# Performance work log

Measured on AMD Instinct MI355X. Metric: run time of the kernel, lower is better.

Reference implementation:

```python
import jax, jax.numpy as jnp
import numpy as np

D_MODEL = 1024
NUM_HEADS = 16
D_K = D_MODEL // NUM_HEADS
TEMPERATURE = 1.0
LN_EPS = 1e-5


def setup_inputs() -> dict:
    key = jax.random.key(0)
    ks = jax.random.split(key, 12)
    B, S, D = 4, 1024, D_MODEL
    w = lambda k: jax.random.normal(k, (D, D), dtype=jnp.float32) * 0.02
    b = lambda k: jax.random.normal(k, (D,), dtype=jnp.float32) * 0.01
    return {
        "query": jax.random.normal(ks[0], (B, S, D), dtype=jnp.float32),
        "key": jax.random.normal(ks[1], (B, S, D), dtype=jnp.float32),
        "value": jax.random.normal(ks[2], (B, S, D), dtype=jnp.float32),
        "wq": w(ks[3]), "bq": b(ks[4]),
        "wk": w(ks[5]), "bk": b(ks[6]),
        "wv": w(ks[7]), "bv": b(ks[8]),
        "wo": w(ks[9]), "bo": b(ks[10]),
        "temporal_bias": jax.random.normal(ks[11], (1, 1, NUM_HEADS, 1, 1), dtype=jnp.float32) * 0.01,
        "adaptive_temp": jnp.ones((1,), dtype=jnp.float32),
        "ln_gamma": jnp.ones((D,), dtype=jnp.float32),
        "ln_beta": jnp.zeros((D,), dtype=jnp.float32),
    }


def reference(query, key, value, wq, bq, wk, bk, wv, bv, wo, bo,
              temporal_bias, adaptive_temp, ln_gamma, ln_beta):
    B, S, D = query.shape
    H, dk = NUM_HEADS, D_K
    # QKV projections -> (B, H, S, dk)
    Q = (query @ wq.T + bq).reshape(B, S, H, dk).transpose(0, 2, 1, 3)
    K = (key @ wk.T + bk).reshape(B, S, H, dk).transpose(0, 2, 1, 3)
    V = (value @ wv.T + bv).reshape(B, S, H, dk).transpose(0, 2, 1, 3)
    scores = jnp.einsum('bhqd,bhkd->bhqk', Q, K) / jnp.sqrt(jnp.float32(dk))
    scores = scores / (TEMPERATURE * adaptive_temp)
    # torch broadcasting bug reproduced: (B,H,S,S) + (1,1,H,1,1) -> (1,B,H,S,S)
    scores5 = scores[None, ...] + temporal_bias  # (1, B, H, S, S)
    attn = jax.nn.softmax(scores5, axis=-1)      # (1, B, H, S, S)
    ctx5 = jnp.einsum('xbhqk,bhkd->xbhqd', attn, V)  # (1, B, H, S, dk)
    # torch: transpose(1,2) -> (1, H, B, S, dk), then view(B, S, D)
    ctx = jnp.swapaxes(ctx5, 1, 2).reshape(B, S, D)
    out = ctx @ wo.T + bo
    y = out + query
    mu = jnp.mean(y, axis=-1, keepdims=True)
    var = jnp.mean(jnp.square(y - mu), axis=-1, keepdims=True)
    out_ln = (y - mu) / jnp.sqrt(var + LN_EPS) * ln_gamma + ln_beta
    return out_ln, attn
```

## Files before the change

kernel.cpp:

```cpp
#include <hip/hip_runtime.h>
#include <math.h>

#define BB 4
#define SS 1024
#define DD 1024
#define HH 16
#define DKK 64
#define NN (BB*SS)
#define LN_EPS 1e-5f
#define QB 64
#define JB 64

typedef __attribute__((ext_vector_type(8))) short bf16x8;
typedef __attribute__((ext_vector_type(4))) float f32x4;
typedef __attribute__((address_space(3))) unsigned int lds_u32;
typedef const __attribute__((address_space(1))) unsigned int glb_u32;

static __device__ __forceinline__ unsigned short f2bf(float x){
    unsigned int u = __float_as_uint(x);
    u += 0x7fff + ((u >> 16) & 1);
    return (unsigned short)(u >> 16);
}
static __device__ __forceinline__ int swzp16(int r){
    return (r & 15) << 4;
}

__global__ __launch_bounds__(256)
void k_cvt_all(const float* __restrict__ q, const float* __restrict__ k,
               const float* __restrict__ v, const float* __restrict__ w0,
               const float* __restrict__ w1, const float* __restrict__ w2,
               const float* __restrict__ w3, unsigned short* __restrict__ xout,
               unsigned short* __restrict__ wout){
    const int bidx = blockIdx.x;
    const float* src; unsigned short* dst; size_t i;
    if (bidx < 6144) {
        const int z = bidx >> 11, bi = bidx & 2047;
        src = (z == 0) ? q : (z == 1) ? k : v;
        dst = xout + (size_t)z*NN*DD;
        i = ((size_t)bi*256 + threadIdx.x)*8;
    } else {
        const int z = (bidx - 6144) >> 9, bi = (bidx - 6144) & 511;
        src = (z == 0) ? w0 : (z == 1) ? w1 : (z == 2) ? w2 : w3;
        dst = wout + (size_t)z*DD*DD;
        i = ((size_t)bi*256 + threadIdx.x)*8;
    }
    float4 a = *reinterpret_cast<const float4*>(&src[i]);
    float4 b = *reinterpret_cast<const float4*>(&src[i+4]);
    int4 w;
    w.x = (int)((unsigned)f2bf(a.x) | ((unsigned)f2bf(a.y) << 16));
    w.y = (int)((unsigned)f2bf(a.z) | ((unsigned)f2bf(a.w) << 16));
    w.z = (int)((unsigned)f2bf(b.x) | ((unsigned)f2bf(b.y) << 16));
    w.w = (int)((unsigned)f2bf(b.z) | ((unsigned)f2bf(b.w) << 16));
    *reinterpret_cast<int4*>(&dst[i]) = w;
}

__global__ __launch_bounds__(256)
void k_gemmqkv(const unsigned short* __restrict__ Xb, const unsigned short* __restrict__ Wb,
               const float* __restrict__ b0, const float* __restrict__ b1,
               const float* __restrict__ b2, unsigned short* __restrict__ outb)
{
    __shared__ __align__(16) unsigned short Als[128*32];
    __shared__ __align__(16) unsigned short Bls[128*32];
    __shared__ __align__(16) unsigned short Cs[128*128];
    const int z = blockIdx.z;
    const unsigned short* X = Xb + (size_t)z*NN*DD;
    const unsigned short* W = Wb + (size_t)z*DD*DD;
    const float* bias = (z == 0) ? b0 : (z == 1) ? b1 : b2;
    unsigned short* out = outb + (size_t)z*NN*DD;

    const int row0 = blockIdx.x * 128;
    const int col0 = blockIdx.y * 128;
    const int t = threadIdx.x;
    const int w = t >> 6, l = t & 63;
    const int wr = w >> 1, wc = w & 1;

    f32x4 acc[4][4];
    #pragma unroll
    for (int m=0;m<4;++m)
        #pragma unroll
        for (int n=0;n<4;++n) acc[m][n] = (f32x4){0.f,0.f,0.f,0.f};

    const int srow  = l >> 2;
    const int skoff = (l & 3) * 8;

    for (int kt = 0; kt < DD; kt += 32) {
        #pragma unroll
        for (int i=0;i<2;++i) {
            const unsigned short* ga = X + (size_t)(row0 + w*32 + i*16 + srow)*DD + kt + skoff;
            const unsigned short* gb = W + (size_t)(col0 + w*32 + i*16 + srow)*DD + kt + skoff;
            __builtin_amdgcn_global_load_lds((glb_u32*)ga, (lds_u32*)&Als[(w*2+i)*512], 16, 0, 0);
            __builtin_amdgcn_global_load_lds((glb_u32*)gb, (lds_u32*)&Bls[(w*2+i)*512], 16, 0, 0);
        }
        __syncthreads();
        bf16x8 af[4], bfr[4];
        #pragma unroll
        for (int m=0;m<4;++m)
            af[m] = *reinterpret_cast<const bf16x8*>(&Als[(wr*64 + m*16 + (l&15))*32 + (l>>4)*8]);
        #pragma unroll
        for (int n=0;n<4;++n)
            bfr[n] = *reinterpret_cast<const bf16x8*>(&Bls[(wc*64 + n*16 + (l&15))*32 + (l>>4)*8]);
        __builtin_amdgcn_s_setprio(1);
        #pragma unroll
        for (int m=0;m<4;++m)
            #pragma unroll
            for (int n=0;n<4;++n)
                acc[m][n] = __builtin_amdgcn_mfma_f32_16x16x32_bf16(af[m], bfr[n], acc[m][n], 0, 0, 0);
        __builtin_amdgcn_s_setprio(0);
        __syncthreads();
    }

    if (z < 2) {
        #pragma unroll
        for (int m=0;m<4;++m){
            const int trb = wr*64 + m*16 + ((l>>4)<<2);
            #pragma unroll
            for (int n=0;n<4;++n){
                const int tc = wc*64 + n*16 + (l&15);
                const float bc = bias[col0 + tc];
                #pragma unroll
                for (int r=0;r<4;++r){
                    const int tr = trb + r;
                    *reinterpret_cast<unsigned short*>(
                        (char*)Cs + ((tr*256 + tc*2) ^ ((tr & 12) << 3))) = f2bf(acc[m][n][r] + bc);
                }
            }
        }
        __syncthreads();
        #pragma unroll
        for (int i=0;i<8;++i){
            const int slot = i*256 + t;
            const int r2 = slot >> 4, g = slot & 15;
            int4 v = *reinterpret_cast<const int4*>(
                (char*)Cs + ((r2*256 + g*16) ^ ((r2 & 12) << 3)));
            *reinterpret_cast<int4*>(&out[(size_t)(row0 + r2)*DD + col0 + g*8]) = v;
        }
    } else {
        #pragma unroll
        for (int m=0;m<4;++m){
            const int trb = wr*64 + m*16 + ((l>>4)<<2);
            #pragma unroll
            for (int n=0;n<4;++n){
                const int tc = wc*64 + n*16 + (l&15);
                const float bc = bias[col0 + tc];
                ushort4 pk;
                pk.x = f2bf(acc[m][n][0] + bc);
                pk.y = f2bf(acc[m][n][1] + bc);
                pk.z = f2bf(acc[m][n][2] + bc);
                pk.w = f2bf(acc[m][n][3] + bc);
                *reinterpret_cast<ushort4*>(
                    (char*)Cs + ((tc*256 + trb*2) ^ ((tc & 15) << 3))) = pk;
            }
        }
        __syncthreads();
        const int b = row0 >> 10;
        const int sbase = row0 & 1023;
        #pragma unroll
        for (int i=0;i<16;++i){
            const int cr = i*8 + (t>>5);
            const int ch = t & 31;
            ushort4 v = *reinterpret_cast<const ushort4*>(
                (char*)Cs + ((cr*256 + ch*8) ^ ((cr & 15) << 3)));
            const int gc = col0 + cr, h = gc >> 6, k = gc & 63;
            *reinterpret_cast<ushort4*>(
                &out[(((size_t)b*HH + h)*DKK + k)*SS + sbase + ch*4]) = v;
        }
    }
}

__global__ __launch_bounds__(512)
void k_attn(const unsigned short* __restrict__ Qb, const unsigned short* __restrict__ Kb,
            const unsigned short* __restrict__ Vtb, const float* __restrict__ at,
            float* __restrict__ attn, unsigned short* __restrict__ ctxb)
{
    __shared__ __align__(16) char SM[147456];
    __shared__ float rsbuf[QB];
    char* Ks   = SM;
    char* Vs   = SM + 8192;
    char* Pall = SM + 16384;
    float* scr = reinterpret_cast<float*>(SM);

    const int f   = blockIdx.x;
    const int wk2 = (f & 7)*128 + (f >> 3);
    const int bh  = wk2 >> 4;
    const int q0  = (wk2 & 15) * QB;
    const int b = bh >> 4, h = bh & 15;
    const int t = threadIdx.x, w = t >> 6, l = t & 63;
    const int g = w & 3;
    const int hf = w >> 2;
    const float alpha = 0.125f / at[0];

    const unsigned short* Qg = Qb  + (size_t)b*SS*DD + (size_t)h*64;
    const unsigned short* Kg = Kb  + (size_t)b*SS*DD + (size_t)h*64;
    const unsigned short* Vg = Vtb + (size_t)bh*DKK*SS;

    const int sj  = t >> 3;
    const int skc = (t & 7) * 8;

    const int qloc = g*16 + (l & 15);

    bf16x8 qf[2];
    #pragma unroll
    for (int ks = 0; ks < 2; ++ks)
        qf[ks] = *reinterpret_cast<const bf16x8*>(
            &Qg[(size_t)(q0 + qloc)*DD + ks*32 + (l>>4)*8]);

    {
        int4 kv = *reinterpret_cast<const int4*>(&Kg[(size_t)sj*DD + skc]);
        int4 vv = *reinterpret_cast<const int4*>(&Vg[(size_t)sj*SS + skc]);
        *reinterpret_cast<int4*>(Ks + ((sj*128 + skc*2) ^ ((sj & 7) << 4))) = kv;
        *reinterpret_cast<int4*>(Vs + ((sj*128 + skc*2) ^ ((sj & 7) << 4))) = vv;
    }
    __syncthreads();

    float srow = 0.f;
    f32x4 cacc[4];
    #pragma unroll
    for (int n = 0; n < 4; ++n) cacc[n] = (f32x4){0.f,0.f,0.f,0.f};

    for (int jt = 0; jt < SS; jt += JB) {
        const bool more = (jt + JB < SS);
        int4 knext, vnext;
        if (more) {
            knext = *reinterpret_cast<const int4*>(&Kg[(size_t)(jt + JB + sj)*DD + skc]);
            vnext = *reinterpret_cast<const int4*>(&Vg[(size_t)sj*SS + jt + JB + skc]);
        }
        f32x4 acc[2];
        #pragma unroll
        for (int n2 = 0; n2 < 2; ++n2) acc[n2] = (f32x4){0.f,0.f,0.f,0.f};
        __builtin_amdgcn_s_setprio(1);
        #pragma unroll
        for (int ks = 0; ks < 2; ++ks) {
            #pragma unroll
            for (int n2 = 0; n2 < 2; ++n2) {
                const int j = (2*hf + n2)*16 + (l & 15);
                bf16x8 kf = *reinterpret_cast<const bf16x8*>(
                    Ks + ((j*128 + (l>>4)*16 + ks*64) ^ ((j & 7) << 4)));
                acc[n2] = __builtin_amdgcn_mfma_f32_16x16x32_bf16(kf, qf[ks], acc[n2], 0, 0, 0);
            }
        }
        __builtin_amdgcn_s_setprio(0);
        #pragma unroll
        for (int n2 = 0; n2 < 2; ++n2) {
            float p0 = __expf(acc[n2][0]*alpha);
            float p1 = __expf(acc[n2][1]*alpha);
            float p2 = __expf(acc[n2][2]*alpha);
            float p3 = __expf(acc[n2][3]*alpha);
            srow += (p0 + p1) + (p2 + p3);
            int2 pk;
            pk.x = (int)((unsigned)f2bf(p0) | ((unsigned)f2bf(p1) << 16));
            pk.y = (int)((unsigned)f2bf(p2) | ((unsigned)f2bf(p3) << 16));
            *reinterpret_cast<int2*>(
                Pall + (size_t)qloc*2048 +
                ((jt*2 + (2*hf + n2)*32 + (l>>4)*8) ^ swzp16(qloc))) = pk;
        }
        __builtin_amdgcn_sched_barrier(0);
        asm volatile("s_waitcnt lgkmcnt(0)" ::: "memory");
        __builtin_amdgcn_sched_barrier(0);
        {
            bf16x8 pf = *reinterpret_cast<const bf16x8*>(
                Pall + (size_t)qloc*2048 +
                ((jt*2 + hf*64 + (l>>4)*16) ^ swzp16(qloc)));
            __builtin_amdgcn_s_setprio(1);
            #pragma unroll
            for (int n = 0; n < 4; ++n) {
                const int d = n*16 + (l & 15);
                bf16x8 vf = *reinterpret_cast<const bf16x8*>(
                    Vs + ((d*128 + (l>>4)*16 + hf*64) ^ ((d & 7) << 4)));
                cacc[n] = __builtin_amdgcn_mfma_f32_16x16x32_bf16(pf, vf, cacc[n], 0, 0, 0);
            }
            __builtin_amdgcn_s_setprio(0);
        }
        __syncthreads();
        if (more) {
            *reinterpret_cast<int4*>(Ks + ((sj*128 + skc*2) ^ ((sj & 7) << 4))) = knext;
            *reinterpret_cast<int4*>(Vs + ((sj*128 + skc*2) ^ ((sj & 7) << 4))) = vnext;
            __syncthreads();
        }
    }

    srow += __shfl_xor(srow, 16, 64);
    srow += __shfl_xor(srow, 32, 64);
    if ((l >> 4) == 0) scr[hf*64 + qloc] = srow;
    __syncthreads();
    const float sinv = 1.0f / (scr[qloc] + scr[64 + qloc]);
    if (hf == 0 && (l >> 4) == 0) rsbuf[qloc] = sinv;
    __syncthreads();

    if (hf == 0) {
        #pragma unroll
        for (int n = 0; n < 4; ++n)
            #pragma unroll
            for (int r = 0; r < 4; ++r)
                scr[(g*64 + l)*16 + n*4 + r] = cacc[n][r];
    }
    __syncthreads();
    if (hf == 1) {
        #pragma unroll
        for (int n = 0; n < 4; ++n) {
            const int d = n*16 + (l & 15);
            #pragma unroll
            for (int r = 0; r < 4; ++r) {
                const float v = (cacc[n][r] + scr[(g*64 + l)*16 + n*4 + r]) * sinv;
                const int q = q0 + g*16 + (l>>4)*4 + r;
                ctxb[(((size_t)h*BB + b)*SS + q)*DKK + d] = f2bf(v);
            }
        }
    }

    #pragma unroll
    for (int i = 0; i < 32; ++i) {
        const int seg = i*32 + (t >> 4);
        const int row = seg >> 4;
        const int cs  = (seg & 15)*64 + (t & 15)*4;
        const float rsv = rsbuf[row];
        int2 u = *reinterpret_cast<const int2*>(
            Pall + (size_t)row*2048 + ((cs*2) ^ swzp16(row)));
        f32x4 fv;
        fv.x = __uint_as_float(((unsigned)u.x) << 16)         * rsv;
        fv.y = __uint_as_float(((unsigned)u.x) & 0xffff0000u) * rsv;
        fv.z = __uint_as_float(((unsigned)u.y) << 16)         * rsv;
        fv.w = __uint_as_float(((unsigned)u.y) & 0xffff0000u) * rsv;
        __builtin_nontemporal_store(fv, reinterpret_cast<f32x4*>(
            &attn[((size_t)bh*SS + q0 + row)*SS + cs]));
    }
}

__global__ __launch_bounds__(256)
void k_gemmo(const unsigned short* __restrict__ X, const unsigned short* __restrict__ W,
             const float* __restrict__ bias, const float* __restrict__ resid,
             float* __restrict__ outf)
{
    __shared__ __align__(16) unsigned short Als[128*32];
    __shared__ __align__(16) unsigned short Bls[128*32];
    const int row0 = blockIdx.x * 128;
    const int col0 = blockIdx.y * 128;
    const int t = threadIdx.x;
    const int w = t >> 6, l = t & 63;
    const int wr = w >> 1, wc = w & 1;

    f32x4 acc[4][4];
    #pragma unroll
    for (int m=0;m<4;++m)
        #pragma unroll
        for (int n=0;n<4;++n) acc[m][n] = (f32x4){0.f,0.f,0.f,0.f};

    const int srow  = l >> 2;
    const int skoff = (l & 3) * 8;

    for (int kt = 0; kt < DD; kt += 32) {
        #pragma unroll
        for (int i=0;i<2;++i) {
            const unsigned short* ga = X + (size_t)(row0 + w*32 + i*16 + srow)*DD + kt + skoff;
            const unsigned short* gb = W + (size_t)(col0 + w*32 + i*16 + srow)*DD + kt + skoff;
            __builtin_amdgcn_global_load_lds((glb_u32*)ga, (lds_u32*)&Als[(w*2+i)*512], 16, 0, 0);
            __builtin_amdgcn_global_load_lds((glb_u32*)gb, (lds_u32*)&Bls[(w*2+i)*512], 16, 0, 0);
        }
        __syncthreads();
        bf16x8 af[4], bfr[4];
        #pragma unroll
        for (int m=0;m<4;++m)
            af[m] = *reinterpret_cast<const bf16x8*>(&Als[(wr*64 + m*16 + (l&15))*32 + (l>>4)*8]);
        #pragma unroll
        for (int n=0;n<4;++n)
            bfr[n] = *reinterpret_cast<const bf16x8*>(&Bls[(wc*64 + n*16 + (l&15))*32 + (l>>4)*8]);
        __builtin_amdgcn_s_setprio(1);
        #pragma unroll
        for (int m=0;m<4;++m)
            #pragma unroll
            for (int n=0;n<4;++n)
                acc[m][n] = __builtin_amdgcn_mfma_f32_16x16x32_bf16(af[m], bfr[n], acc[m][n], 0, 0, 0);
        __builtin_amdgcn_s_setprio(0);
        __syncthreads();
    }

    #pragma unroll
    for (int m=0;m<4;++m){
        const int grow_base = row0 + wr*64 + m*16 + ((l>>4)<<2);
        #pragma unroll
        for (int n=0;n<4;++n){
            const int col = col0 + wc*64 + n*16 + (l&15);
            const float bc = bias[col];
            #pragma unroll
            for (int r=0;r<4;++r){
                const int row = grow_base + r;
                outf[(size_t)row*DD + col] = acc[m][n][r] + bc + resid[(size_t)row*DD + col];
            }
        }
    }
}

__global__ __launch_bounds__(256)
void k_ln(const float* __restrict__ y, const float* __restrict__ g,
          const float* __restrict__ be, float* __restrict__ out)
{
    const int row = blockIdx.x;
    const int t = threadIdx.x;
    float4 v = *reinterpret_cast<const float4*>(&y[(size_t)row*DD + t*4]);
    float s  = v.x + v.y + v.z + v.w;
    float ss = v.x*v.x + v.y*v.y + v.z*v.z + v.w*v.w;
    #pragma unroll
    for (int off = 32; off > 0; off >>= 1) {
        s  += __shfl_xor(s,  off, 64);
        ss += __shfl_xor(ss, off, 64);
    }
    __shared__ float red[8];
    const int lane = t & 63, wid = t >> 6;
    if (lane == 0) { red[wid] = s; red[4+wid] = ss; }
    __syncthreads();
    const float S1 = red[0]+red[1]+red[2]+red[3];
    const float S2 = red[4]+red[5]+red[6]+red[7];
    const float mu  = S1 * (1.0f/DD);
    const float var = fmaxf(S2 * (1.0f/DD) - mu*mu, 0.0f);
    const float rstd = rsqrtf(var + LN_EPS);
    float4 gv = *reinterpret_cast<const float4*>(&g[t*4]);
    float4 bv = *reinterpret_cast<const float4*>(&be[t*4]);
    float4 o;
    o.x = (v.x - mu)*rstd*gv.x + bv.x;
    o.y = (v.y - mu)*rstd*gv.y + bv.y;
    o.z = (v.z - mu)*rstd*gv.z + bv.z;
    o.w = (v.w - mu)*rstd*gv.w + bv.w;
    *reinterpret_cast<float4*>(&out[(size_t)row*DD + t*4]) = o;
}

extern "C" void kernel_launch(void* const* d_in, const int* in_sizes, int n_in,
                              void* d_out, int out_size, void* d_ws, size_t ws_size,
                              hipStream_t stream) {
    const float* query = (const float*)d_in[0];
    const float* key   = (const float*)d_in[1];
    const float* value = (const float*)d_in[2];
    const float* wq = (const float*)d_in[3];
    const float* bq = (const float*)d_in[4];
    const float* wk = (const float*)d_in[5];
    const float* bk = (const float*)d_in[6];
    const float* wv = (const float*)d_in[7];
    const float* bv = (const float*)d_in[8];
    const float* wo = (const float*)d_in[9];
    const float* bo = (const float*)d_in[10];
    const float* at = (const float*)d_in[12];
    const float* g  = (const float*)d_in[13];
    const float* be = (const float*)d_in[14];

    float* out_ln = (float*)d_out;
    float* attn   = (float*)d_out + (size_t)NN*DD;

    char* wsb = (char*)d_ws;
    unsigned short* xq   = (unsigned short*)(wsb);
    unsigned short* Qb   = (unsigned short*)(wsb + ((size_t)24<<20));
    unsigned short* Kb   = (unsigned short*)(wsb + ((size_t)32<<20));
    unsigned short* Vtb  = (unsigned short*)(wsb + ((size_t)40<<20));
    unsigned short* ctxb = (unsigned short*)(wsb + ((size_t)48<<20));
    unsigned short* wqb  = (unsigned short*)(wsb + ((size_t)56<<20));
    float*          y    = (float*)(wsb);

    k_cvt_all<<<8192, 256, 0, stream>>>(query, key, value, wq, wk, wv, wo, xq, wqb);

    k_gemmqkv<<<dim3(32, 8, 3), 256, 0, stream>>>(xq, wqb, bq, bk, bv, Qb);

    k_attn<<<dim3(1024), 512, 0, stream>>>(Qb, Kb, Vtb, at, attn, ctxb);

    k_gemmo<<<dim3(32, 8), 256, 0, stream>>>(ctxb, wqb + (size_t)3*DD*DD, bo, query, y);

    k_ln<<<NN, 256, 0, stream>>>(y, g, be, out_ln);
}
```

Baseline: 210.8 us.

## Restructure attention into two-pass recompute softmax without shared memory

Replaces the single-pass attention kernel, which kept the whole 64x1024 probability tile in 144KB of LDS, with a two-pass scheme. The first pass computes QK^T only to accumulate row sums; the second pass recomputes the scores, writes normalized probabilities straight to global memory, and moves them into the PV MFMA operand layout with warp shuffles. K and V are now read directly from global/L2 without LDS staging, and the block size drops to 256 threads. This trades doubled QK^T compute and extra global loads for no LDS use, higher occupancy, and no block-level barriers.

```diff
diff --git a/kernel.cpp b/kernel.cpp
--- a/kernel.cpp
+++ b/kernel.cpp
@@ -8,7 +8,6 @@
 #define DKK 64
 #define NN (BB*SS)
 #define LN_EPS 1e-5f
-#define QB 64
 #define JB 64
 
 typedef __attribute__((ext_vector_type(8))) short bf16x8;
@@ -20,9 +19,6 @@
     unsigned int u = __float_as_uint(x);
     u += 0x7fff + ((u >> 16) & 1);
     return (unsigned short)(u >> 16);
-}
-static __device__ __forceinline__ int swzp16(int r){
-    return (r & 15) << 4;
 }
 
 __global__ __launch_bounds__(256)
@@ -167,161 +163,124 @@
     }
 }
 
-__global__ __launch_bounds__(512)
+__global__ __launch_bounds__(256)
 void k_attn(const unsigned short* __restrict__ Qb, const unsigned short* __restrict__ Kb,
             const unsigned short* __restrict__ Vtb, const float* __restrict__ at,
             float* __restrict__ attn, unsigned short* __restrict__ ctxb)
 {
-    __shared__ __align__(16) char SM[147456];
-    __shared__ float rsbuf[QB];
-    char* Ks   = SM;
-    char* Vs   = SM + 8192;
-    char* Pall = SM + 16384;
-    float* scr = reinterpret_cast<float*>(SM);
-
     const int f   = blockIdx.x;
     const int wk2 = (f & 7)*128 + (f >> 3);
     const int bh  = wk2 >> 4;
-    const int q0  = (wk2 & 15) * QB;
+    const int q0  = (wk2 & 15) * 64;
     const int b = bh >> 4, h = bh & 15;
     const int t = threadIdx.x, w = t >> 6, l = t & 63;
-    const int g = w & 3;
-    const int hf = w >> 2;
+    const int lq = l & 15;
+    const int c  = l >> 4;
+    const int qg = q0 + w*16;
     const float alpha = 0.125f / at[0];
 
     const unsigned short* Qg = Qb  + (size_t)b*SS*DD + (size_t)h*64;
     const unsigned short* Kg = Kb  + (size_t)b*SS*DD + (size_t)h*64;
     const unsigned short* Vg = Vtb + (size_t)bh*DKK*SS;
 
-    const int sj  = t >> 3;
-    const int skc = (t & 7) * 8;
-
-    const int qloc = g*16 + (l & 15);
-
     bf16x8 qf[2];
     #pragma unroll
     for (int ks = 0; ks < 2; ++ks)
         qf[ks] = *reinterpret_cast<const bf16x8*>(
-            &Qg[(size_t)(q0 + qloc)*DD + ks*32 + (l>>4)*8]);
-
-    {
-        int4 kv = *reinterpret_cast<const int4*>(&Kg[(size_t)sj*DD + skc]);
-        int4 vv = *reinterpret_cast<const int4*>(&Vg[(size_t)sj*SS + skc]);
-        *reinterpret_cast<int4*>(Ks + ((sj*128 + skc*2) ^ ((sj & 7) << 4))) = kv;
-        *reinterpret_cast<int4*>(Vs + ((sj*128 + skc*2) ^ ((sj & 7) << 4))) = vv;
-    }
-    __syncthreads();
+            &Qg[(size_t)(qg + lq)*DD + ks*32 + c*8]);
 
     float srow = 0.f;
-    f32x4 cacc[4];
-    #pragma unroll
-    for (int n = 0; n < 4; ++n) cacc[n] = (f32x4){0.f,0.f,0.f,0.f};
-
     for (int jt = 0; jt < SS; jt += JB) {
-        const bool more = (jt + JB < SS);
-        int4 knext, vnext;
-        if (more) {
-            knext = *reinterpret_cast<const int4*>(&Kg[(size_t)(jt + JB + sj)*DD + skc]);
-            vnext = *reinterpret_cast<const int4*>(&Vg[(size_t)sj*SS + jt + JB + skc]);
-        }
-        f32x4 acc[2];
-        #pragma unroll
-        for (int n2 = 0; n2 < 2; ++n2) acc[n2] = (f32x4){0.f,0.f,0.f,0.f};
-        __builtin_amdgcn_s_setprio(1);
+        f32x4 acc[4];
+        #pragma unroll
+        for (int n = 0; n < 4; ++n) acc[n] = (f32x4){0.f,0.f,0.f,0.f};
         #pragma unroll
         for (int ks = 0; ks < 2; ++ks) {
             #pragma unroll
-            for (int n2 = 0; n2 < 2; ++n2) {
-                const int j = (2*hf + n2)*16 + (l & 15);
+            for (int n = 0; n < 4; ++n) {
                 bf16x8 kf = *reinterpret_cast<const bf16x8*>(
-                    Ks + ((j*128 + (l>>4)*16 + ks*64) ^ ((j & 7) << 4)));
-                acc[n2] = __builtin_amdgcn_mfma_f32_16x16x32_bf16(kf, qf[ks], acc[n2], 0, 0, 0);
-            }
-        }
-        __builtin_amdgcn_s_setprio(0);
-        #pragma unroll
-        for (int n2 = 0; n2 < 2; ++n2) {
-            float p0 = __expf(acc[n2][0]*alpha);
-            float p1 = __expf(acc[n2][1]*alpha);
-            float p2 = __expf(acc[n2][2]*alpha);
-            float p3 = __expf(acc[n2][3]*alpha);
-            srow += (p0 + p1) + (p2 + p3);
-            int2 pk;
-            pk.x = (int)((unsigned)f2bf(p0) | ((unsigned)f2bf(p1) << 16));
-            pk.y = (int)((unsigned)f2bf(p2) | ((unsigned)f2bf(p3) << 16));
-            *reinterpret_cast<int2*>(
-                Pall + (size_t)qloc*2048 +
-                ((jt*2 + (2*hf + n2)*32 + (l>>4)*8) ^ swzp16(qloc))) = pk;
-        }
-        __builtin_amdgcn_sched_barrier(0);
-        asm volatile("s_waitcnt lgkmcnt(0)" ::: "memory");
-        __builtin_amdgcn_sched_barrier(0);
-        {
-            bf16x8 pf = *reinterpret_cast<const bf16x8*>(
-                Pall + (size_t)qloc*2048 +
-                ((jt*2 + hf*64 + (l>>4)*16) ^ swzp16(qloc)));
-            __builtin_amdgcn_s_setprio(1);
-            #pragma unroll
-            for (int n = 0; n < 4; ++n) {
-                const int d = n*16 + (l & 15);
-                bf16x8 vf = *reinterpret_cast<const bf16x8*>(
-                    Vs + ((d*128 + (l>>4)*16 + hf*64) ^ ((d & 7) << 4)));
-                cacc[n] = __builtin_amdgcn_mfma_f32_16x16x32_bf16(pf, vf, cacc[n], 0, 0, 0);
-            }
-            __builtin_amdgcn_s_setprio(0);
-        }
-        __syncthreads();
-        if (more) {
-            *reinterpret_cast<int4*>(Ks + ((sj*128 + skc*2) ^ ((sj & 7) << 4))) = knext;
-            *reinterpret_cast<int4*>(Vs + ((sj*128 + skc*2) ^ ((sj & 7) << 4))) = vnext;
-            __syncthreads();
-        }
-    }
-
+                    &Kg[(size_t)(jt + n*16 + lq)*DD + ks*32 + c*8]);
+                acc[n] = __builtin_amdgcn_mfma_f32_16x16x32_bf16(kf, qf[ks], acc[n], 0, 0, 0);
+            }
+        }
+        #pragma unroll
+        for (int n = 0; n < 4; ++n) {
+            srow += __expf(acc[n][0]*alpha) + __expf(acc[n][1]*alpha)
+                  + __expf(acc[n][2]*alpha) + __expf(acc[n][3]*alpha);
+        }
+    }
     srow += __shfl_xor(srow, 16, 64);
     srow += __shfl_xor(srow, 32, 64);
-    if ((l >> 4) == 0) scr[hf*64 + qloc] = srow;
-    __syncthreads();
-    const float sinv = 1.0f / (scr[qloc] + scr[64 + qloc]);
-    if (hf == 0 && (l >> 4) == 0) rsbuf[qloc] = sinv;
-    __syncthreads();
-
-    if (hf == 0) {
-        #pragma unroll
-        for (int n = 0; n < 4; ++n)
-            #pragma unroll
-            for (int r = 0; r < 4; ++r)
-                scr[(g*64 + l)*16 + n*4 + r] = cacc[n][r];
-    }
-    __syncthreads();
-    if (hf == 1) {
+    const float sinv = 1.0f / srow;
+
+    f32x4 cacc[4];
+    #pragma unroll
+    for (int dg = 0; dg < 4; ++dg) cacc[dg] = (f32x4){0.f,0.f,0.f,0.f};
+
+    const int lA = lq + ((2*c) & 3)*16;
+    const int lB = lq + ((2*c + 1) & 3)*16;
+    const bool hi = (c >> 1) != 0;
+
+    for (int jt = 0; jt < SS; jt += JB) {
+        f32x4 acc[4];
+        #pragma unroll
+        for (int n = 0; n < 4; ++n) acc[n] = (f32x4){0.f,0.f,0.f,0.f};
+        #pragma unroll
+        for (int ks = 0; ks < 2; ++ks) {
+            #pragma unroll
+            for (int n = 0; n < 4; ++n) {
+                bf16x8 kf = *reinterpret_cast<const bf16x8*>(
+                    &Kg[(size_t)(jt + n*16 + lq)*DD + ks*32 + c*8]);
+                acc[n] = __builtin_amdgcn_mfma_f32_16x16x32_bf16(kf, qf[ks], acc[n], 0, 0, 0);
+            }
+        }
+        unsigned pka[4], pkb[4];
         #pragma unroll
         for (int n = 0; n < 4; ++n) {
-            const int d = n*16 + (l & 15);
-            #pragma unroll
-            for (int r = 0; r < 4; ++r) {
-                const float v = (cacc[n][r] + scr[(g*64 + l)*16 + n*4 + r]) * sinv;
-                const int q = q0 + g*16 + (l>>4)*4 + r;
-                ctxb[(((size_t)h*BB + b)*SS + q)*DKK + d] = f2bf(v);
-            }
-        }
-    }
-
-    #pragma unroll
-    for (int i = 0; i < 32; ++i) {
-        const int seg = i*32 + (t >> 4);
-        const int row = seg >> 4;
-        const int cs  = (seg & 15)*64 + (t & 15)*4;
-        const float rsv = rsbuf[row];
-        int2 u = *reinterpret_cast<const int2*>(
-            Pall + (size_t)row*2048 + ((cs*2) ^ swzp16(row)));
-        f32x4 fv;
-        fv.x = __uint_as_float(((unsigned)u.x) << 16)         * rsv;
-        fv.y = __uint_as_float(((unsigned)u.x) & 0xffff0000u) * rsv;
-        fv.z = __uint_as_float(((unsigned)u.y) << 16)         * rsv;
-        fv.w = __uint_as_float(((unsigned)u.y) & 0xffff0000u) * rsv;
-        __builtin_nontemporal_store(fv, reinterpret_cast<f32x4*>(
-            &attn[((size_t)bh*SS + q0 + row)*SS + cs]));
+            float p0 = __expf(acc[n][0]*alpha) * sinv;
+            float p1 = __expf(acc[n][1]*alpha) * sinv;
+            float p2 = __expf(acc[n][2]*alpha) * sinv;
+            float p3 = __expf(acc[n][3]*alpha) * sinv;
+            f32x4 fv = (f32x4){p0, p1, p2, p3};
+            *reinterpret_cast<f32x4*>(
+                &attn[((size_t)bh*SS + qg + lq)*SS + jt + n*16 + c*4]) = fv;
+            pka[n] = (unsigned)f2bf(p0) | ((unsigned)f2bf(p1) << 16);
+            pkb[n] = (unsigned)f2bf(p2) | ((unsigned)f2bf(p3) << 16);
+        }
+        #pragma unroll
+        for (int t2 = 0; t2 < 2; ++t2) {
+            const int n0 = 2*t2, n1 = 2*t2 + 1;
+            unsigned a0 = (unsigned)__shfl((int)pka[n0], lA, 64);
+            unsigned a1 = (unsigned)__shfl((int)pka[n1], lA, 64);
+            unsigned b0 = (unsigned)__shfl((int)pkb[n0], lA, 64);
+            unsigned b1 = (unsigned)__shfl((int)pkb[n1], lA, 64);
+            unsigned c0 = (unsigned)__shfl((int)pka[n0], lB, 64);
+            unsigned c1 = (unsigned)__shfl((int)pka[n1], lB, 64);
+            unsigned d0 = (unsigned)__shfl((int)pkb[n0], lB, 64);
+            unsigned d1 = (unsigned)__shfl((int)pkb[n1], lB, 64);
+            int4 uu;
+            uu.x = (int)(hi ? a1 : a0);
+            uu.y = (int)(hi ? b1 : b0);
+            uu.z = (int)(hi ? c1 : c0);
+            uu.w = (int)(hi ? d1 : d0);
+            bf16x8 pf = *reinterpret_cast<const bf16x8*>(&uu);
+            #pragma unroll
+            for (int dg = 0; dg < 4; ++dg) {
+                bf16x8 vf = *reinterpret_cast<const bf16x8*>(
+                    &Vg[(size_t)(dg*16 + lq)*SS + jt + t2*32 + c*8]);
+                cacc[dg] = __builtin_amdgcn_mfma_f32_16x16x32_bf16(pf, vf, cacc[dg], 0, 0, 0);
+            }
+        }
+    }
+
+    #pragma unroll
+    for (int dg = 0; dg < 4; ++dg) {
+        const int d = dg*16 + lq;
+        #pragma unroll
+        for (int r = 0; r < 4; ++r) {
+            const int qrow = qg + 4*c + r;
+            ctxb[(((size_t)h*BB + b)*SS + qrow)*DKK + d] = f2bf(cacc[dg][r]);
+        }
     }
 }
 
@@ -456,7 +415,7 @@
 
     k_gemmqkv<<<dim3(32, 8, 3), 256, 0, stream>>>(xq, wqb, bq, bk, bv, Qb);
 
-    k_attn<<<dim3(1024), 512, 0, stream>>>(Qb, Kb, Vtb, at, attn, ctxb);
+    k_attn<<<dim3(1024), 256, 0, stream>>>(Qb, Kb, Vtb, at, attn, ctxb);
 
     k_gemmo<<<dim3(32, 8), 256, 0, stream>>>(ctxb, wqb + (size_t)3*DD*DD, bo, query, y);
 
```

Result: slower. 295.6 us (+40.2%).
